# Optimization experiments

Hardware: AMD Instinct MI355X
Metric: run time of the kernel (lower is better)

## Reference

```python
import jax, jax.numpy as jnp
from jax import lax
import numpy as np

NUM_NODES = 32
C = 64
EPS = 1e-5

# Static random DAG: edge i->j (i<j) with prob 0.25; node index == topological order.
_rng = np.random.default_rng(0)
_adj = _rng.random((NUM_NODES, NUM_NODES)) < 0.25
PRED = [tuple(i for i in range(j) if _adj[i, j]) for j in range(NUM_NODES)]
SUCC = [tuple(j for j in range(i + 1, NUM_NODES) if _adj[i, j]) for i in range(NUM_NODES)]
ISPAN = [max(s) if s else NUM_NODES for s in SUCC]
# Nodes whose outputs survive the torch live/delete bookkeeping at the final stack:
# sinks (ispan == NUM_NODES) plus predecessors of the last topological node.
FINAL = [i for i in range(NUM_NODES) if ISPAN[i] >= NUM_NODES - 1]


def _sep_conv(y, dw, pw, stride):
    # depthwise 3x3 (torch padding=1) then pointwise 1x1
    y = lax.conv_general_dilated(y, dw, (stride, stride), ((1, 1), (1, 1)),
                                 feature_group_count=C,
                                 dimension_numbers=('NCHW', 'OIHW', 'NCHW'))
    return jnp.einsum('oc,nchw->nohw', pw, y)


def _bn(y, g, b, m, v):
    inv = (g / jnp.sqrt(v + EPS))[None, :, None, None]
    return (y - m[None, :, None, None]) * inv + b[None, :, None, None]


def _forward(x, dw, pw, gamma, beta, mean, var, agg_w):
    outs = [None] * NUM_NODES
    for i in range(NUM_NODES):  # static structural loop over the fixed DAG
        preds = PRED[i]
        if len(preds) == 0:          # input node: consumes x, downsample stride 2
            y, stride = x, 2
        elif len(preds) == 1:        # single predecessor: plain pass-through (squeeze)
            y, stride = outs[preds[0]], 1
        else:                         # sigmoid-weighted sum of predecessor outputs
            w = jax.nn.sigmoid(agg_w[i, :len(preds)])
            y = jnp.einsum('pnchw,p->nchw', jnp.stack([outs[p] for p in preds]), w)
            stride = 1
        h = _sep_conv(jax.nn.relu(y), dw[i], pw[i], stride)
        outs[i] = _bn(h, gamma[i], beta[i], mean[i], var[i])
    return jnp.mean(jnp.stack([outs[i] for i in FINAL]), axis=0)


def setup_inputs():
    key = jax.random.key(0)
    ks = jax.random.split(key, 8)
    B, H, W = 8, 112, 112
    x = jax.random.normal(ks[0], (B, C, H, W), jnp.float32)
    # fan-in scaling keeps activations bounded across the up-to-32-deep DAG
    dw = jax.random.normal(ks[1], (NUM_NODES, C, 1, 3, 3), jnp.float32) / 3.0
    pw = jax.random.normal(ks[2], (NUM_NODES, C, C), jnp.float32) / 8.0
    gamma = jax.random.uniform(ks[3], (NUM_NODES, C), jnp.float32, 0.5, 1.5)
    beta = jax.random.normal(ks[4], (NUM_NODES, C), jnp.float32) * 0.1
    mean = jax.random.normal(ks[5], (NUM_NODES, C), jnp.float32) * 0.1
    var = jax.random.uniform(ks[6], (NUM_NODES, C), jnp.float32, 0.5, 1.5)
    agg_w = jax.random.normal(ks[7], (NUM_NODES, NUM_NODES), jnp.float32)
    return {"x": x, "dw": dw, "pw": pw, "gamma": gamma, "beta": beta,
            "mean": mean, "var": var, "agg_w": agg_w}


def reference(x, dw, pw, gamma, beta, mean, var, agg_w):
    return _forward(x, dw, pw, gamma, beta, mean, var, agg_w)
```

## Files before the change

### kernel.cpp

```cpp
#include <hip/hip_runtime.h>
#include <cstdint>
#include <cstddef>

#define NN 32
#define NODE_ELEMS 1605632

typedef unsigned __int128 u128;
typedef __attribute__((ext_vector_type(8))) short bf16x8;
typedef __attribute__((ext_vector_type(4))) float f32x4;

static void compute_adj(bool adj[NN][NN]) {
  uint32_t pool[4];
  uint32_t hc = 0x43b0d7e5u;
  auto hashmix = [&hc](uint32_t v) -> uint32_t {
    v ^= hc; hc *= 0x931e8875u; v *= hc; v ^= v >> 16; return v;
  };
  auto mix = [](uint32_t x, uint32_t y) -> uint32_t {
    uint32_t r = x * 0xca01f9ddu - y * 0x4973f715u; r ^= r >> 16; return r;
  };
  for (int i = 0; i < 4; i++) pool[i] = hashmix(0u);
  for (int s = 0; s < 4; s++)
    for (int d = 0; d < 4; d++)
      if (s != d) pool[d] = mix(pool[d], hashmix(pool[s]));
  uint32_t hb = 0x8b51f9ddu;
  uint32_t w[8];
  for (int k = 0; k < 8; k++) {
    uint32_t v = pool[k & 3];
    v ^= hb; hb *= 0x58f38dedu; v *= hb; v ^= v >> 16;
    w[k] = v;
  }
  uint64_t s64[4];
  for (int j = 0; j < 4; j++) s64[j] = (uint64_t)w[2 * j] | ((uint64_t)w[2 * j + 1] << 32);
  u128 initstate = ((u128)s64[0] << 64) | s64[1];
  u128 initseq   = ((u128)s64[2] << 64) | s64[3];
  const u128 MULT = ((u128)0x2360ED051FC65DA4ULL << 64) | 0x4385DF649FCCF645ULL;
  u128 state = 0;
  u128 inc = (initseq << 1) | 1;
  state = state * MULT + inc;
  state += initstate;
  state = state * MULT + inc;
  for (int i = 0; i < NN; i++)
    for (int j = 0; j < NN; j++) {
      state = state * MULT + inc;
      uint64_t hi = (uint64_t)(state >> 64), lo = (uint64_t)state;
      unsigned rot = (unsigned)(hi >> 58);
      uint64_t xr = hi ^ lo;
      uint64_t out = (xr >> rot) | (xr << ((64u - rot) & 63u));
      double dv = (double)(out >> 11) * (1.0 / 9007199254740992.0);
      adj[i][j] = (dv < 0.25);
    }
}

struct NodeDesc {
  uint8_t node, npred, slot, flags;
  uint8_t pred_slot[31];
  uint8_t pad;
};
struct GroupArg { int n; NodeDesc d[32]; };
struct FinalArg { int nf; uint8_t slot[32]; };

__device__ __forceinline__ float bf2f_lo(unsigned int w) {
  union { unsigned int u; float f; } c; c.u = w << 16; return c.f;
}
__device__ __forceinline__ float bf2f_hi(unsigned int w) {
  union { unsigned int u; float f; } c; c.u = w & 0xFFFF0000u; return c.f;
}
__device__ __forceinline__ float bf2f(unsigned short h) {
  union { unsigned int u; float f; } c; c.u = ((unsigned int)h) << 16; return c.f;
}
__device__ __forceinline__ unsigned short f2bf(float f) {
  union { float f; unsigned int u; } c; c.f = f;
  unsigned int u = c.u + 0x7FFFu + ((c.u >> 16) & 1u);
  return (unsigned short)(u >> 16);
}

__global__ void prep_kernel(const float* __restrict__ pwall,
                            const float* __restrict__ aggw,
                            unsigned short* __restrict__ pwswz,
                            float* __restrict__ wsig) {
  int i = blockIdx.x * 256 + threadIdx.x;
  if (i < NN * 4096) {
    int cc = i & 63, o = (i >> 6) & 63;
    int base = i & ~4095;
    pwswz[base + o * 64 + ((((cc >> 3) ^ (o & 7)) << 3) | (cc & 7))] = f2bf(pwall[i]);
  } else {
    int j = i - NN * 4096;
    if (j < NN * NN) wsig[j] = 1.f / (1.f + expf(-aggw[j]));
  }
}

__global__ __launch_bounds__(256) void input_kernel(
    GroupArg g,
    const float* __restrict__ x,
    const float* __restrict__ dwall,
    const unsigned short* __restrict__ pwswz,
    const float* __restrict__ gmall,
    const float* __restrict__ btall,
    const float* __restrict__ mnall,
    const float* __restrict__ vrall,
    unsigned short* __restrict__ wsb)
{
  __shared__ float xtile[5 * 17 * 64];
  __shared__ __align__(16) unsigned short tbuf[1024];

  const int b = blockIdx.x & 7;
  const int m = blockIdx.x >> 3;
  const int t = threadIdx.x;
  const int ty = (m / 7) * 2;
  const int tx = (m % 7) * 8;

  const int dwc = t & 63;
  const int pbase = (t >> 6) * 4;

  {
    const int r0 = t >> 6;
    const float* xb = x + (size_t)(b * 64 + dwc) * 12544;
    const int iy0 = ty * 2 - 1;
    const int xbase = tx * 2 - 4;
    for (int iyL = r0; iyL < 5; iyL += 4) {
      int gy = iy0 + iyL;
      bool rowok = ((unsigned)gy < 112u);
      const float* row = xb + gy * 112 + xbase;
      float4 z = make_float4(0.f, 0.f, 0.f, 0.f);
      float4 v0 = z, v1 = z, v2 = z, v3 = z, v4 = z;
      if (rowok) {
        if (xbase >= 0) v0 = *(const float4*)(row);
        v1 = *(const float4*)(row + 4);
        v2 = *(const float4*)(row + 8);
        v3 = *(const float4*)(row + 12);
        v4 = *(const float4*)(row + 16);
      }
      float* dst = xtile + (iyL * 17) * 64 + dwc;
      dst[0 * 64]  = fmaxf(v0.w, 0.f);
      dst[1 * 64]  = fmaxf(v1.x, 0.f);
      dst[2 * 64]  = fmaxf(v1.y, 0.f);
      dst[3 * 64]  = fmaxf(v1.z, 0.f);
      dst[4 * 64]  = fmaxf(v1.w, 0.f);
      dst[5 * 64]  = fmaxf(v2.x, 0.f);
      dst[6 * 64]  = fmaxf(v2.y, 0.f);
      dst[7 * 64]  = fmaxf(v2.z, 0.f);
      dst[8 * 64]  = fmaxf(v2.w, 0.f);
      dst[9 * 64]  = fmaxf(v3.x, 0.f);
      dst[10 * 64] = fmaxf(v3.y, 0.f);
      dst[11 * 64] = fmaxf(v3.z, 0.f);
      dst[12 * 64] = fmaxf(v3.w, 0.f);
      dst[13 * 64] = fmaxf(v4.x, 0.f);
      dst[14 * 64] = fmaxf(v4.y, 0.f);
      dst[15 * 64] = fmaxf(v4.z, 0.f);
      dst[16 * 64] = fmaxf(v4.w, 0.f);
    }
  }

  const int lane = t & 63;
  const int wave = t >> 6;
  const int lm = lane & 15;
  const int quad = lane >> 4;
  const int oc = wave * 16 + lm;

  float kk9[9];
  {
    const float* k9 = dwall + (g.d[0].node * 64 + dwc) * 9;
    #pragma unroll
    for (int q = 0; q < 9; q++) kk9[q] = k9[q];
  }

  for (int kk = 0; kk < g.n; kk++) {
    const NodeDesc nd = g.d[kk];
    const int node = nd.node;

    __syncthreads();

    const unsigned short* pwn = pwswz + node * 4096;
    bf16x8 bfrag[2];
    #pragma unroll
    for (int ks = 0; ks < 2; ks++) {
      int gg = ks * 4 + quad;
      bfrag[ks] = *(const bf16x8*)&pwn[oc * 64 + ((gg ^ (oc & 7)) << 3)];
    }

    float tv[4];
    #pragma unroll
    for (int jj = 0; jj < 4; jj++) {
      int p = pbase + jj;
      int py = p >> 3, px = p & 7;
      const float* r0 = xtile + ((py * 2) * 17 + px * 2) * 64 + dwc;
      tv[jj] = r0[0]    * kk9[0] + r0[64]   * kk9[1] + r0[128]  * kk9[2]
             + r0[1088] * kk9[3] + r0[1152] * kk9[4] + r0[1216] * kk9[5]
             + r0[2176] * kk9[6] + r0[2240] * kk9[7] + r0[2304] * kk9[8];
    }

    #pragma unroll
    for (int jj = 0; jj < 4; jj++) {
      int p = pbase + jj;
      tbuf[p * 64 + ((((dwc >> 3) ^ (p & 7)) << 3) | (dwc & 7))] = f2bf(tv[jj]);
    }

    float nk9[9];
    if (kk + 1 < g.n) {
      const float* k9 = dwall + (g.d[kk + 1].node * 64 + dwc) * 9;
      #pragma unroll
      for (int q = 0; q < 9; q++) nk9[q] = k9[q];
    }

    __syncthreads();

    bf16x8 afrag[2];
    #pragma unroll
    for (int ks = 0; ks < 2; ks++) {
      int pos = lm;
      int gg = ks * 4 + quad;
      afrag[ks] = *(const bf16x8*)&tbuf[pos * 64 + ((gg ^ (pos & 7)) << 3)];
    }
    f32x4 acc = (f32x4){0.f, 0.f, 0.f, 0.f};
    #pragma unroll
    for (int ks = 0; ks < 2; ks++)
      acc = __builtin_amdgcn_mfma_f32_16x16x32_bf16(afrag[ks], bfrag[ks], acc, 0, 0, 0);

    unsigned short* slotp = wsb + (size_t)nd.slot * NODE_ELEMS;
    {
      int gi = node * 64 + oc;
      float inv = gmall[gi] / sqrtf(vrall[gi] + 1e-5f);
      float mn = mnall[gi], btv = btall[gi];
      #pragma unroll
      for (int rr = 0; rr < 4; rr++) {
        int pos = quad * 4 + rr;
        int gy = ty + (pos >> 3), gx = tx + (pos & 7);
        size_t base = (((size_t)(b * 56 + gy)) * 56 + gx) * 64 + oc;
        slotp[base] = f2bf((acc[rr] - mn) * inv + btv);
      }
    }

    if (kk + 1 < g.n) {
      #pragma unroll
      for (int q = 0; q < 9; q++) kk9[q] = nk9[q];
    }
  }
}

__global__ __launch_bounds__(256) void level_kernel(
    GroupArg g,
    const float* __restrict__ dwall,
    const unsigned short* __restrict__ pwswz,
    const float* __restrict__ gmall,
    const float* __restrict__ btall,
    const float* __restrict__ mnall,
    const float* __restrict__ vrall,
    const float* __restrict__ wsig,
    unsigned short* __restrict__ wsb)
{
  __shared__ float smem[3840];
  __shared__ __align__(16) unsigned short tbuf[2048];

  const int bid = blockIdx.x;
  const int nid = bid / 784;
  const int r   = bid - nid * 784;
  const int b = r & 7;
  const int m = r >> 3;
  const int t = threadIdx.x;
  const int ty = (m / 7) * 4;
  const int tx = (m % 7) * 8;

  const NodeDesc nd = g.d[nid];
  const int node = nd.node;

  const int dwc = t & 63;
  const int pbase = (t >> 6) * 8;

  const int lane = t & 63;
  const int wave = t >> 6;
  const int mtile = wave & 1;
  const int npair = wave >> 1;
  const int lm = lane & 15;
  const int quad = lane >> 4;
  const unsigned short* pwn = pwswz + node * 4096;
  bf16x8 bfrag[2][2];
  #pragma unroll
  for (int nt = 0; nt < 2; nt++) {
    int oc = (npair * 2 + nt) * 16 + lm;
    #pragma unroll
    for (int ks = 0; ks < 2; ks++) {
      int gg = ks * 4 + quad;
      bfrag[nt][ks] = *(const bf16x8*)&pwn[oc * 64 + ((gg ^ (oc & 7)) << 3)];
    }
  }

  const float* k9 = dwall + (node * 64 + dwc) * 9;
  float kk9[9];
  #pragma unroll
  for (int q = 0; q < 9; q++) kk9[q] = k9[q];

  const int np = nd.npred;
  float sa[2][8];
  int off[2];
  bool inb[2];
  #pragma unroll
  for (int u = 0; u < 2; u++) {
    int idx = t + u * 256;
    bool valid = (u == 0) || (t < 224);
    int pos = idx >> 3, q8 = idx & 7;
    int hy = pos / 10, hx = pos - hy * 10;
    int gy = ty + hy - 1, gx = tx + hx - 1;
    inb[u] = valid && ((unsigned)gy < 56u) && ((unsigned)gx < 56u);
    off[u] = ((b * 56 + gy) * 56 + gx) * 64 + q8 * 8;
    #pragma unroll
    for (int q = 0; q < 8; q++) sa[u][q] = 0.f;
  }
  for (int p0 = 0; p0 < np; p0 += 4) {
    uint4 v[4][2];
    #pragma unroll
    for (int pp = 0; pp < 4; pp++) {
      if (p0 + pp < np) {
        const unsigned short* pb = wsb + (size_t)nd.pred_slot[p0 + pp] * NODE_ELEMS;
        #pragma unroll
        for (int u = 0; u < 2; u++)
          if (inb[u]) v[pp][u] = *(const uint4*)(pb + off[u]);
      }
    }
    float wv4[4];
    #pragma unroll
    for (int pp = 0; pp < 4; pp++)
      if (p0 + pp < np)
        wv4[pp] = (np == 1) ? 1.0f : wsig[node * 32 + p0 + pp];
    #pragma unroll
    for (int pp = 0; pp < 4; pp++) {
      if (p0 + pp < np) {
        float wv = wv4[pp];
        #pragma unroll
        for (int u = 0; u < 2; u++) {
          if (inb[u]) {
            sa[u][0] = fmaf(wv, bf2f_lo(v[pp][u].x), sa[u][0]);
            sa[u][1] = fmaf(wv, bf2f_hi(v[pp][u].x), sa[u][1]);
            sa[u][2] = fmaf(wv, bf2f_lo(v[pp][u].y), sa[u][2]);
            sa[u][3] = fmaf(wv, bf2f_hi(v[pp][u].y), sa[u][3]);
            sa[u][4] = fmaf(wv, bf2f_lo(v[pp][u].z), sa[u][4]);
            sa[u][5] = fmaf(wv, bf2f_hi(v[pp][u].z), sa[u][5]);
            sa[u][6] = fmaf(wv, bf2f_lo(v[pp][u].w), sa[u][6]);
            sa[u][7] = fmaf(wv, bf2f_hi(v[pp][u].w), sa[u][7]);
          }
        }
      }
    }
  }
  #pragma unroll
  for (int u = 0; u < 2; u++) {
    int idx = t + u * 256;
    if ((u == 0) || (t < 224)) {
      float4 s0 = make_float4(fmaxf(sa[u][0], 0.f), fmaxf(sa[u][1], 0.f),
                              fmaxf(sa[u][2], 0.f), fmaxf(sa[u][3], 0.f));
      float4 s1 = make_float4(fmaxf(sa[u][4], 0.f), fmaxf(sa[u][5], 0.f),
                              fmaxf(sa[u][6], 0.f), fmaxf(sa[u][7], 0.f));
      *(float4*)&smem[idx * 8] = s0;
      *(float4*)&smem[idx * 8 + 4] = s1;
    }
  }
  __syncthreads();
  float tv[8];
  #pragma unroll
  for (int jj = 0; jj < 8; jj++) {
    int p = pbase + jj;
    int py = p >> 3, px = p & 7;
    const float* r0 = smem + (py * 10 + px) * 64 + dwc;
    tv[jj] = r0[0]    * kk9[0] + r0[64]   * kk9[1] + r0[128]  * kk9[2]
           + r0[640]  * kk9[3] + r0[704]  * kk9[4] + r0[768]  * kk9[5]
           + r0[1280] * kk9[6] + r0[1344] * kk9[7] + r0[1408] * kk9[8];
  }

  #pragma unroll
  for (int jj = 0; jj < 8; jj++) {
    int p = pbase + jj;
    tbuf[p * 64 + ((((dwc >> 3) ^ (p & 7)) << 3) | (dwc & 7))] = f2bf(tv[jj]);
  }
  __syncthreads();

  bf16x8 afrag[2];
  #pragma unroll
  for (int ks = 0; ks < 2; ks++) {
    int pos = mtile * 16 + lm;
    int gg = ks * 4 + quad;
    afrag[ks] = *(const bf16x8*)&tbuf[pos * 64 + ((gg ^ (pos & 7)) << 3)];
  }
  f32x4 acc[2];
  #pragma unroll
  for (int nt = 0; nt < 2; nt++) {
    acc[nt] = (f32x4){0.f, 0.f, 0.f, 0.f};
    #pragma unroll
    for (int ks = 0; ks < 2; ks++)
      acc[nt] = __builtin_amdgcn_mfma_f32_16x16x32_bf16(afrag[ks], bfrag[nt][ks], acc[nt], 0, 0, 0);
  }

  unsigned short* slotp = wsb + (size_t)nd.slot * NODE_ELEMS;
  #pragma unroll
  for (int nt = 0; nt < 2; nt++) {
    int oc = (npair * 2 + nt) * 16 + lm;
    int gi = node * 64 + oc;
    float inv = gmall[gi] / sqrtf(vrall[gi] + 1e-5f);
    float mn = mnall[gi], btv = btall[gi];
    #pragma unroll
    for (int rr = 0; rr < 4; rr++) {
      int pos = mtile * 16 + quad * 4 + rr;
      int gy = ty + (pos >> 3), gx = tx + (pos & 7);
      size_t base = (((size_t)(b * 56 + gy)) * 56 + gx) * 64 + oc;
      slotp[base] = f2bf((acc[nt][rr] - mn) * inv + btv);
    }
  }
}

__global__ __launch_bounds__(256) void chain_kernel(
    GroupArg g,
    const float* __restrict__ dwall,
    const unsigned short* __restrict__ pwswz,
    const float* __restrict__ gmall,
    const float* __restrict__ btall,
    const float* __restrict__ mnall,
    const float* __restrict__ vrall,
    const float* __restrict__ wsig,
    unsigned short* __restrict__ wsb)
{
  __shared__ float smem[2560];
  __shared__ __align__(16) unsigned short tbuf[1024];

  const int bid = blockIdx.x;
  const int b = bid & 7;
  const int m = bid >> 3;
  const int t = threadIdx.x;
  const int ty = (m / 7) * 2;
  const int tx = (m % 7) * 8;

  const NodeDesc nd = g.d[0];
  const int node = nd.node;

  const int dwc = t & 63;
  const int pbase = (t >> 6) * 4;

  const int lane = t & 63;
  const int wave = t >> 6;
  const int lm = lane & 15;
  const int quad = lane >> 4;
  const int oc = wave * 16 + lm;
  const unsigned short* pwn = pwswz + node * 4096;
  bf16x8 bfrag[2];
  #pragma unroll
  for (int ks = 0; ks < 2; ks++) {
    int gg = ks * 4 + quad;
    bfrag[ks] = *(const bf16x8*)&pwn[oc * 64 + ((gg ^ (oc & 7)) << 3)];
  }

  const float* k9 = dwall + (node * 64 + dwc) * 9;
  float kk9[9];
  #pragma unroll
  for (int q = 0; q < 9; q++) kk9[q] = k9[q];

  const int np = nd.npred;
  float sa[2][8];
  int off[2];
  bool inb[2];
  #pragma unroll
  for (int u = 0; u < 2; u++) {
    int idx = t + u * 256;
    bool valid = (u == 0) || (t < 64);
    int pos = idx >> 3, q8 = idx & 7;
    int hy = pos / 10, hx = pos - hy * 10;
    int gy = ty + hy - 1, gx = tx + hx - 1;
    inb[u] = valid && ((unsigned)gy < 56u) && ((unsigned)gx < 56u);
    off[u] = ((b * 56 + gy) * 56 + gx) * 64 + q8 * 8;
    #pragma unroll
    for (int q = 0; q < 8; q++) sa[u][q] = 0.f;
  }
  for (int p0 = 0; p0 < np; p0 += 4) {
    uint4 v[4][2];
    #pragma unroll
    for (int pp = 0; pp < 4; pp++) {
      if (p0 + pp < np) {
        const unsigned short* pb = wsb + (size_t)nd.pred_slot[p0 + pp] * NODE_ELEMS;
        #pragma unroll
        for (int u = 0; u < 2; u++)
          if (inb[u]) v[pp][u] = *(const uint4*)(pb + off[u]);
      }
    }
    float wv4[4];
    #pragma unroll
    for (int pp = 0; pp < 4; pp++)
      if (p0 + pp < np)
        wv4[pp] = (np == 1) ? 1.0f : wsig[node * 32 + p0 + pp];
    #pragma unroll
    for (int pp = 0; pp < 4; pp++) {
      if (p0 + pp < np) {
        float wv = wv4[pp];
        #pragma unroll
        for (int u = 0; u < 2; u++) {
          if (inb[u]) {
            sa[u][0] = fmaf(wv, bf2f_lo(v[pp][u].x), sa[u][0]);
            sa[u][1] = fmaf(wv, bf2f_hi(v[pp][u].x), sa[u][1]);
            sa[u][2] = fmaf(wv, bf2f_lo(v[pp][u].y), sa[u][2]);
            sa[u][3] = fmaf(wv, bf2f_hi(v[pp][u].y), sa[u][3]);
            sa[u][4] = fmaf(wv, bf2f_lo(v[pp][u].z), sa[u][4]);
            sa[u][5] = fmaf(wv, bf2f_hi(v[pp][u].z), sa[u][5]);
            sa[u][6] = fmaf(wv, bf2f_lo(v[pp][u].w), sa[u][6]);
            sa[u][7] = fmaf(wv, bf2f_hi(v[pp][u].w), sa[u][7]);
          }
        }
      }
    }
  }
  #pragma unroll
  for (int u = 0; u < 2; u++) {
    int idx = t + u * 256;
    if ((u == 0) || (t < 64)) {
      float4 s0 = make_float4(fmaxf(sa[u][0], 0.f), fmaxf(sa[u][1], 0.f),
                              fmaxf(sa[u][2], 0.f), fmaxf(sa[u][3], 0.f));
      float4 s1 = make_float4(fmaxf(sa[u][4], 0.f), fmaxf(sa[u][5], 0.f),
                              fmaxf(sa[u][6], 0.f), fmaxf(sa[u][7], 0.f));
      *(float4*)&smem[idx * 8] = s0;
      *(float4*)&smem[idx * 8 + 4] = s1;
    }
  }
  __syncthreads();
  float tv[4];
  #pragma unroll
  for (int jj = 0; jj < 4; jj++) {
    int p = pbase + jj;
    int py = p >> 3, px = p & 7;
    const float* r0 = smem + (py * 10 + px) * 64 + dwc;
    tv[jj] = r0[0]    * kk9[0] + r0[64]   * kk9[1] + r0[128]  * kk9[2]
           + r0[640]  * kk9[3] + r0[704]  * kk9[4] + r0[768]  * kk9[5]
           + r0[1280] * kk9[6] + r0[1344] * kk9[7] + r0[1408] * kk9[8];
  }

  #pragma unroll
  for (int jj = 0; jj < 4; jj++) {
    int p = pbase + jj;
    tbuf[p * 64 + ((((dwc >> 3) ^ (p & 7)) << 3) | (dwc & 7))] = f2bf(tv[jj]);
  }
  __syncthreads();

  bf16x8 afrag[2];
  #pragma unroll
  for (int ks = 0; ks < 2; ks++) {
    int pos = lm;
    int gg = ks * 4 + quad;
    afrag[ks] = *(const bf16x8*)&tbuf[pos * 64 + ((gg ^ (pos & 7)) << 3)];
  }
  f32x4 acc = (f32x4){0.f, 0.f, 0.f, 0.f};
  #pragma unroll
  for (int ks = 0; ks < 2; ks++)
    acc = __builtin_amdgcn_mfma_f32_16x16x32_bf16(afrag[ks], bfrag[ks], acc, 0, 0, 0);

  unsigned short* slotp = wsb + (size_t)nd.slot * NODE_ELEMS;
  {
    int gi = node * 64 + oc;
    float inv = gmall[gi] / sqrtf(vrall[gi] + 1e-5f);
    float mn = mnall[gi], btv = btall[gi];
    #pragma unroll
    for (int rr = 0; rr < 4; rr++) {
      int pos = quad * 4 + rr;
      int gy = ty + (pos >> 3), gx = tx + (pos & 7);
      size_t base = (((size_t)(b * 56 + gy)) * 56 + gx) * 64 + oc;
      slotp[base] = f2bf((acc[rr] - mn) * inv + btv);
    }
  }
}

__global__ __launch_bounds__(256) void finalize_kernel(
    FinalArg fa, const unsigned short* __restrict__ wsb,
    float* __restrict__ out, float inv_nf)
{
  __shared__ float lds[64 * 29];
  const int bid = blockIdx.x;
  const int half = bid & 1;
  const int by = bid >> 1;
  const int b = by / 56, y = by - b * 56;
  const int x0 = half * 28;
  const size_t rbase = ((((size_t)b * 56 + y) * 56) + x0) * 64;
  const int t = threadIdx.x;
  const int nf = fa.nf;

  if (t < 224) {
    const int xx = t >> 3, q8 = t & 7;
    const unsigned short* p0 = wsb + rbase + xx * 64 + q8 * 8;
    float s0 = 0.f, s1 = 0.f, s2 = 0.f, s3 = 0.f,
          s4 = 0.f, s5 = 0.f, s6 = 0.f, s7 = 0.f;
    for (int f0 = 0; f0 < nf; f0 += 4) {
      uint4 va, vb, vc, vd;
      if (f0 + 0 < nf) va = *(const uint4*)(p0 + (size_t)fa.slot[f0 + 0] * NODE_ELEMS);
      if (f0 + 1 < nf) vb = *(const uint4*)(p0 + (size_t)fa.slot[f0 + 1] * NODE_ELEMS);
      if (f0 + 2 < nf) vc = *(const uint4*)(p0 + (size_t)fa.slot[f0 + 2] * NODE_ELEMS);
      if (f0 + 3 < nf) vd = *(const uint4*)(p0 + (size_t)fa.slot[f0 + 3] * NODE_ELEMS);
      if (f0 + 0 < nf) {
        s0 += bf2f_lo(va.x); s1 += bf2f_hi(va.x); s2 += bf2f_lo(va.y); s3 += bf2f_hi(va.y);
        s4 += bf2f_lo(va.z); s5 += bf2f_hi(va.z); s6 += bf2f_lo(va.w); s7 += bf2f_hi(va.w);
      }
      if (f0 + 1 < nf) {
        s0 += bf2f_lo(vb.x); s1 += bf2f_hi(vb.x); s2 += bf2f_lo(vb.y); s3 += bf2f_hi(vb.y);
        s4 += bf2f_lo(vb.z); s5 += bf2f_hi(vb.z); s6 += bf2f_lo(vb.w); s7 += bf2f_hi(vb.w);
      }
      if (f0 + 2 < nf) {
        s0 += bf2f_lo(vc.x); s1 += bf2f_hi(vc.x); s2 += bf2f_lo(vc.y); s3 += bf2f_hi(vc.y);
        s4 += bf2f_lo(vc.z); s5 += bf2f_hi(vc.z); s6 += bf2f_lo(vc.w); s7 += bf2f_hi(vc.w);
      }
      if (f0 + 3 < nf) {
        s0 += bf2f_lo(vd.x); s1 += bf2f_hi(vd.x); s2 += bf2f_lo(vd.y); s3 += bf2f_hi(vd.y);
        s4 += bf2f_lo(vd.z); s5 += bf2f_hi(vd.z); s6 += bf2f_lo(vd.w); s7 += bf2f_hi(vd.w);
      }
    }
    float* dl = lds + (q8 * 8) * 29 + xx;
    dl[0 * 29] = s0 * inv_nf; dl[1 * 29] = s1 * inv_nf;
    dl[2 * 29] = s2 * inv_nf; dl[3 * 29] = s3 * inv_nf;
    dl[4 * 29] = s4 * inv_nf; dl[5 * 29] = s5 * inv_nf;
    dl[6 * 29] = s6 * inv_nf; dl[7 * 29] = s7 * inv_nf;
  }
  __syncthreads();
  float* dst = out + (size_t)b * 64 * 3136 + (size_t)y * 56 + x0;
  for (int j = t; j < 1792; j += 256) {
    int c = j / 28, xx = j - c * 28;
    dst[(size_t)c * 3136 + xx] = lds[c * 29 + xx];
  }
}

extern "C" void kernel_launch(void* const* d_in, const int* in_sizes, int n_in,
                              void* d_out, int out_size, void* d_ws, size_t ws_size,
                              hipStream_t stream) {
  (void)in_sizes; (void)n_in; (void)ws_size; (void)out_size;
  const float* x     = (const float*)d_in[0];
  const float* dw    = (const float*)d_in[1];
  const float* pw    = (const float*)d_in[2];
  const float* gamma = (const float*)d_in[3];
  const float* beta  = (const float*)d_in[4];
  const float* mean  = (const float*)d_in[5];
  const float* var   = (const float*)d_in[6];
  const float* aggw  = (const float*)d_in[7];
  unsigned short* wsb = (unsigned short*)d_ws;
  float* out = (float*)d_out;

  bool adj[NN][NN];
  compute_adj(adj);

  int npred[NN], preds[NN][NN], nsucc[NN], ispan[NN], level[NN];
  for (int j = 0; j < NN; j++) {
    npred[j] = 0;
    for (int i = 0; i < j; i++) if (adj[i][j]) preds[j][npred[j]++] = i;
  }
  for (int i = 0; i < NN; i++) {
    nsucc[i] = 0; ispan[i] = NN;
    int mx = -1;
    for (int j = i + 1; j < NN; j++) if (adj[i][j]) { nsucc[i]++; mx = j; }
    if (nsucc[i] > 0) ispan[i] = mx;
  }
  int maxlev = 0;
  for (int j = 0; j < NN; j++) {
    int lv = 0;
    for (int p = 0; p < npred[j]; p++) {
      int cand = level[preds[j][p]] + 1;
      if (cand > lv) lv = cand;
    }
    level[j] = lv;
    if (lv > maxlev) maxlev = lv;
  }
  bool isfinal[NN]; int nf = 0;
  for (int i = 0; i < NN; i++) { isfinal[i] = (ispan[i] >= NN - 1); if (isfinal[i]) nf++; }
  int lastlvl[NN];
  for (int i = 0; i < NN; i++) {
    lastlvl[i] = -1;
    for (int j = i + 1; j < NN; j++) if (adj[i][j] && level[j] > lastlvl[i]) lastlvl[i] = level[j];
  }
  int slot[NN]; bool used[NN];
  for (int s = 0; s < NN; s++) used[s] = false;
  for (int L = 0; L <= maxlev; L++) {
    for (int i = 0; i < NN; i++) {
      if (level[i] != L) continue;
      int s = 0; while (used[s]) s++;
      used[s] = true; slot[i] = s;
    }
    for (int i = 0; i < NN; i++)
      if (level[i] <= L && !isfinal[i] && lastlvl[i] == L)
        used[slot[i]] = false;
  }
  int maxs = 0;
  for (int i = 0; i < NN; i++) if (slot[i] > maxs) maxs = slot[i];

  unsigned short* pwswz = wsb + (size_t)(maxs + 1) * NODE_ELEMS;
  float* wsig = (float*)(pwswz + NN * 4096);

  float inv_nf = 1.0f / (float)nf;

  prep_kernel<<<516, 256, 0, stream>>>(pw, aggw, pwswz, wsig);

  for (int L = 0; L <= maxlev; L++) {
    GroupArg g; g.n = 0;
    for (int i = 0; i < NN; i++) {
      if (level[i] != L) continue;
      NodeDesc& nd = g.d[g.n++];
      nd.node = (uint8_t)i;
      nd.npred = (uint8_t)npred[i];
      nd.slot = (uint8_t)slot[i];
      nd.flags = 0;
      for (int p = 0; p < npred[i]; p++) nd.pred_slot[p] = (uint8_t)slot[preds[i][p]];
    }
    if (g.n > 0) {
      if (L == 0) {
        input_kernel<<<1568, 256, 0, stream>>>(g, x, dw, pwswz, gamma, beta,
                                               mean, var, wsb);
      } else if (g.n == 1) {
        chain_kernel<<<1568, 256, 0, stream>>>(g, dw, pwswz, gamma, beta,
                                               mean, var, wsig, wsb);
      } else {
        level_kernel<<<784 * g.n, 256, 0, stream>>>(g, dw, pwswz, gamma, beta,
                                                    mean, var, wsig, wsb);
      }
    }
  }

  FinalArg fa; fa.nf = 0;
  for (int i = 0; i < NN; i++) if (isfinal[i]) fa.slot[fa.nf++] = (uint8_t)slot[i];
  finalize_kernel<<<896, 256, 0, stream>>>(fa, wsb, out, inv_nf);
}
```

Before: 222.9 us.

## Fuse last DAG node computation with final mean-stack into one kernel

When the deepest level has a single node and that node is a final output, the new kernel computes that node and immediately averages it with the other final node outputs, writing NCHW fp32 output directly. This removes one kernel launch, plus the write and re-read of the last node's activation through global memory. In exchange the fused kernel's output writes are scattered 8-wide tile rows instead of 28-wide rows. The finalize loop is also simplified from 4-way unrolled loads to a plain loop.

```diff
diff --git a/kernel.cpp b/kernel.cpp
--- a/kernel.cpp
+++ b/kernel.cpp
@@ -560,6 +560,196 @@
   }
 }
 
+__global__ __launch_bounds__(256) void chain_final_kernel(
+    GroupArg g, FinalArg fa, int fself,
+    const float* __restrict__ dwall,
+    const unsigned short* __restrict__ pwswz,
+    const float* __restrict__ gmall,
+    const float* __restrict__ btall,
+    const float* __restrict__ mnall,
+    const float* __restrict__ vrall,
+    const float* __restrict__ wsig,
+    const unsigned short* __restrict__ wsb,
+    float* __restrict__ out, float inv_nf)
+{
+  __shared__ float smem[2560];
+  __shared__ __align__(16) unsigned short tbuf[1024];
+
+  const int bid = blockIdx.x;
+  const int b = bid & 7;
+  const int m = bid >> 3;
+  const int t = threadIdx.x;
+  const int ty = (m / 7) * 2;
+  const int tx = (m % 7) * 8;
+
+  const NodeDesc nd = g.d[0];
+  const int node = nd.node;
+
+  const int dwc = t & 63;
+  const int pbase = (t >> 6) * 4;
+
+  const int lane = t & 63;
+  const int wave = t >> 6;
+  const int lm = lane & 15;
+  const int quad = lane >> 4;
+  const int oc = wave * 16 + lm;
+  const unsigned short* pwn = pwswz + node * 4096;
+  bf16x8 bfrag[2];
+  #pragma unroll
+  for (int ks = 0; ks < 2; ks++) {
+    int gg = ks * 4 + quad;
+    bfrag[ks] = *(const bf16x8*)&pwn[oc * 64 + ((gg ^ (oc & 7)) << 3)];
+  }
+
+  const float* k9 = dwall + (node * 64 + dwc) * 9;
+  float kk9[9];
+  #pragma unroll
+  for (int q = 0; q < 9; q++) kk9[q] = k9[q];
+
+  const int np = nd.npred;
+  float sa[2][8];
+  int off[2];
+  bool inb[2];
+  #pragma unroll
+  for (int u = 0; u < 2; u++) {
+    int idx = t + u * 256;
+    bool valid = (u == 0) || (t < 64);
+    int pos = idx >> 3, q8 = idx & 7;
+    int hy = pos / 10, hx = pos - hy * 10;
+    int gy = ty + hy - 1, gx = tx + hx - 1;
+    inb[u] = valid && ((unsigned)gy < 56u) && ((unsigned)gx < 56u);
+    off[u] = ((b * 56 + gy) * 56 + gx) * 64 + q8 * 8;
+    #pragma unroll
+    for (int q = 0; q < 8; q++) sa[u][q] = 0.f;
+  }
+  for (int p0 = 0; p0 < np; p0 += 4) {
+    uint4 v[4][2];
+    #pragma unroll
+    for (int pp = 0; pp < 4; pp++) {
+      if (p0 + pp < np) {
+        const unsigned short* pb = wsb + (size_t)nd.pred_slot[p0 + pp] * NODE_ELEMS;
+        #pragma unroll
+        for (int u = 0; u < 2; u++)
+          if (inb[u]) v[pp][u] = *(const uint4*)(pb + off[u]);
+      }
+    }
+    float wv4[4];
+    #pragma unroll
+    for (int pp = 0; pp < 4; pp++)
+      if (p0 + pp < np)
+        wv4[pp] = (np == 1) ? 1.0f : wsig[node * 32 + p0 + pp];
+    #pragma unroll
+    for (int pp = 0; pp < 4; pp++) {
+      if (p0 + pp < np) {
+        float wv = wv4[pp];
+        #pragma unroll
+        for (int u = 0; u < 2; u++) {
+          if (inb[u]) {
+            sa[u][0] = fmaf(wv, bf2f_lo(v[pp][u].x), sa[u][0]);
+            sa[u][1] = fmaf(wv, bf2f_hi(v[pp][u].x), sa[u][1]);
+            sa[u][2] = fmaf(wv, bf2f_lo(v[pp][u].y), sa[u][2]);
+            sa[u][3] = fmaf(wv, bf2f_hi(v[pp][u].y), sa[u][3]);
+            sa[u][4] = fmaf(wv, bf2f_lo(v[pp][u].z), sa[u][4]);
+            sa[u][5] = fmaf(wv, bf2f_hi(v[pp][u].z), sa[u][5]);
+            sa[u][6] = fmaf(wv, bf2f_lo(v[pp][u].w), sa[u][6]);
+            sa[u][7] = fmaf(wv, bf2f_hi(v[pp][u].w), sa[u][7]);
+          }
+        }
+      }
+    }
+  }
+  #pragma unroll
+  for (int u = 0; u < 2; u++) {
+    int idx = t + u * 256;
+    if ((u == 0) || (t < 64)) {
+      float4 s0 = make_float4(fmaxf(sa[u][0], 0.f), fmaxf(sa[u][1], 0.f),
+                              fmaxf(sa[u][2], 0.f), fmaxf(sa[u][3], 0.f));
+      float4 s1 = make_float4(fmaxf(sa[u][4], 0.f), fmaxf(sa[u][5], 0.f),
+                              fmaxf(sa[u][6], 0.f), fmaxf(sa[u][7], 0.f));
+      *(float4*)&smem[idx * 8] = s0;
+      *(float4*)&smem[idx * 8 + 4] = s1;
+    }
+  }
+  __syncthreads();
+  float tv[4];
+  #pragma unroll
+  for (int jj = 0; jj < 4; jj++) {
+    int p = pbase + jj;
+    int py = p >> 3, px = p & 7;
+    const float* r0 = smem + (py * 10 + px) * 64 + dwc;
+    tv[jj] = r0[0]    * kk9[0] + r0[64]   * kk9[1] + r0[128]  * kk9[2]
+           + r0[640]  * kk9[3] + r0[704]  * kk9[4] + r0[768]  * kk9[5]
+           + r0[1280] * kk9[6] + r0[1344] * kk9[7] + r0[1408] * kk9[8];
+  }
+
+  #pragma unroll
+  for (int jj = 0; jj < 4; jj++) {
+    int p = pbase + jj;
+    tbuf[p * 64 + ((((dwc >> 3) ^ (p & 7)) << 3) | (dwc & 7))] = f2bf(tv[jj]);
+  }
+  __syncthreads();
+
+  bf16x8 afrag[2];
+  #pragma unroll
+  for (int ks = 0; ks < 2; ks++) {
+    int pos = lm;
+    int gg = ks * 4 + quad;
+    afrag[ks] = *(const bf16x8*)&tbuf[pos * 64 + ((gg ^ (pos & 7)) << 3)];
+  }
+  f32x4 acc = (f32x4){0.f, 0.f, 0.f, 0.f};
+  #pragma unroll
+  for (int ks = 0; ks < 2; ks++)
+    acc = __builtin_amdgcn_mfma_f32_16x16x32_bf16(afrag[ks], bfrag[ks], acc, 0, 0, 0);
+
+  unsigned short own[4];
+  {
+    int gi = node * 64 + oc;
+    float inv = gmall[gi] / sqrtf(vrall[gi] + 1e-5f);
+    float mn = mnall[gi], btv = btall[gi];
+    #pragma unroll
+    for (int rr = 0; rr < 4; rr++)
+      own[rr] = f2bf((acc[rr] - mn) * inv + btv);
+  }
+  __syncthreads();
+  #pragma unroll
+  for (int rr = 0; rr < 4; rr++)
+    tbuf[(quad * 4 + rr) * 64 + oc] = own[rr];
+  __syncthreads();
+
+  if (t < 128) {
+    int pos = t >> 3, q8 = t & 7;
+    int gy = ty + (pos >> 3), gx = tx + (pos & 7);
+    size_t base = (((size_t)(b * 56 + gy)) * 56 + gx) * 64 + q8 * 8;
+    float s0 = 0.f, s1 = 0.f, s2 = 0.f, s3 = 0.f,
+          s4 = 0.f, s5 = 0.f, s6 = 0.f, s7 = 0.f;
+    for (int f = 0; f < fa.nf; f++) {
+      if (f == fself) {
+        const unsigned short* op = &tbuf[pos * 64 + q8 * 8];
+        s0 += bf2f(op[0]); s1 += bf2f(op[1]); s2 += bf2f(op[2]); s3 += bf2f(op[3]);
+        s4 += bf2f(op[4]); s5 += bf2f(op[5]); s6 += bf2f(op[6]); s7 += bf2f(op[7]);
+      } else {
+        uint4 v = *(const uint4*)(wsb + (size_t)fa.slot[f] * NODE_ELEMS + base);
+        s0 += bf2f_lo(v.x); s1 += bf2f_hi(v.x); s2 += bf2f_lo(v.y); s3 += bf2f_hi(v.y);
+        s4 += bf2f_lo(v.z); s5 += bf2f_hi(v.z); s6 += bf2f_lo(v.w); s7 += bf2f_hi(v.w);
+      }
+    }
+    float* fb = smem + (q8 * 8) * 17 + pos;
+    fb[0 * 17] = s0 * inv_nf; fb[1 * 17] = s1 * inv_nf;
+    fb[2 * 17] = s2 * inv_nf; fb[3 * 17] = s3 * inv_nf;
+    fb[4 * 17] = s4 * inv_nf; fb[5 * 17] = s5 * inv_nf;
+    fb[6 * 17] = s6 * inv_nf; fb[7 * 17] = s7 * inv_nf;
+  }
+  __syncthreads();
+  {
+    float* dst = out + (size_t)b * 64 * 3136;
+    for (int j = t; j < 1024; j += 256) {
+      int c = j >> 4, pos = j & 15;
+      int gy = ty + (pos >> 3), gx = tx + (pos & 7);
+      dst[(size_t)c * 3136 + gy * 56 + gx] = smem[c * 17 + pos];
+    }
+  }
+}
+
 __global__ __launch_bounds__(256) void finalize_kernel(
     FinalArg fa, const unsigned short* __restrict__ wsb,
     float* __restrict__ out, float inv_nf)
@@ -579,28 +769,10 @@
     const unsigned short* p0 = wsb + rbase + xx * 64 + q8 * 8;
     float s0 = 0.f, s1 = 0.f, s2 = 0.f, s3 = 0.f,
           s4 = 0.f, s5 = 0.f, s6 = 0.f, s7 = 0.f;
-    for (int f0 = 0; f0 < nf; f0 += 4) {
-      uint4 va, vb, vc, vd;
-      if (f0 + 0 < nf) va = *(const uint4*)(p0 + (size_t)fa.slot[f0 + 0] * NODE_ELEMS);
-      if (f0 + 1 < nf) vb = *(const uint4*)(p0 + (size_t)fa.slot[f0 + 1] * NODE_ELEMS);
-      if (f0 + 2 < nf) vc = *(const uint4*)(p0 + (size_t)fa.slot[f0 + 2] * NODE_ELEMS);
-      if (f0 + 3 < nf) vd = *(const uint4*)(p0 + (size_t)fa.slot[f0 + 3] * NODE_ELEMS);
-      if (f0 + 0 < nf) {
-        s0 += bf2f_lo(va.x); s1 += bf2f_hi(va.x); s2 += bf2f_lo(va.y); s3 += bf2f_hi(va.y);
-        s4 += bf2f_lo(va.z); s5 += bf2f_hi(va.z); s6 += bf2f_lo(va.w); s7 += bf2f_hi(va.w);
-      }
-      if (f0 + 1 < nf) {
-        s0 += bf2f_lo(vb.x); s1 += bf2f_hi(vb.x); s2 += bf2f_lo(vb.y); s3 += bf2f_hi(vb.y);
-        s4 += bf2f_lo(vb.z); s5 += bf2f_hi(vb.z); s6 += bf2f_lo(vb.w); s7 += bf2f_hi(vb.w);
-      }
-      if (f0 + 2 < nf) {
-        s0 += bf2f_lo(vc.x); s1 += bf2f_hi(vc.x); s2 += bf2f_lo(vc.y); s3 += bf2f_hi(vc.y);
-        s4 += bf2f_lo(vc.z); s5 += bf2f_hi(vc.z); s6 += bf2f_lo(vc.w); s7 += bf2f_hi(vc.w);
-      }
-      if (f0 + 3 < nf) {
-        s0 += bf2f_lo(vd.x); s1 += bf2f_hi(vd.x); s2 += bf2f_lo(vd.y); s3 += bf2f_hi(vd.y);
-        s4 += bf2f_lo(vd.z); s5 += bf2f_hi(vd.z); s6 += bf2f_lo(vd.w); s7 += bf2f_hi(vd.w);
-      }
+    for (int f = 0; f < nf; f++) {
+      uint4 v = *(const uint4*)(p0 + (size_t)fa.slot[f] * NODE_ELEMS);
+      s0 += bf2f_lo(v.x); s1 += bf2f_hi(v.x); s2 += bf2f_lo(v.y); s3 += bf2f_hi(v.y);
+      s4 += bf2f_lo(v.z); s5 += bf2f_hi(v.z); s6 += bf2f_lo(v.w); s7 += bf2f_hi(v.w);
     }
     float* dl = lds + (q8 * 8) * 29 + xx;
     dl[0 * 29] = s0 * inv_nf; dl[1 * 29] = s1 * inv_nf;
@@ -682,6 +854,16 @@
 
   float inv_nf = 1.0f / (float)nf;
 
+  int lastN = -1, lastCount = 0;
+  for (int i = 0; i < NN; i++) if (level[i] == maxlev) { lastN = i; lastCount++; }
+  bool fuse = (maxlev >= 1) && (lastCount == 1) && isfinal[lastN];
+  FinalArg fa; fa.nf = 0; int fself = -1;
+  for (int i = 0; i < NN; i++) if (isfinal[i]) {
+    if (i == lastN) fself = fa.nf;
+    fa.slot[fa.nf++] = (uint8_t)slot[i];
+  }
+  if (fself < 0) fuse = false;
+
   prep_kernel<<<516, 256, 0, stream>>>(pw, aggw, pwswz, wsig);
 
   for (int L = 0; L <= maxlev; L++) {
@@ -699,6 +881,10 @@
       if (L == 0) {
         input_kernel<<<1568, 256, 0, stream>>>(g, x, dw, pwswz, gamma, beta,
                                                mean, var, wsb);
+      } else if (L == maxlev && fuse) {
+        chain_final_kernel<<<1568, 256, 0, stream>>>(g, fa, fself, dw, pwswz,
+                                                     gamma, beta, mean, var,
+                                                     wsig, wsb, out, inv_nf);
       } else if (g.n == 1) {
         chain_kernel<<<1568, 256, 0, stream>>>(g, dw, pwswz, gamma, beta,
                                                mean, var, wsig, wsb);
@@ -709,7 +895,7 @@
     }
   }
 
-  FinalArg fa; fa.nf = 0;
-  for (int i = 0; i < NN; i++) if (isfinal[i]) fa.slot[fa.nf++] = (uint8_t)slot[i];
-  finalize_kernel<<<896, 256, 0, stream>>>(fa, wsb, out, inv_nf);
-}
+  if (!fuse) {
+    finalize_kernel<<<896, 256, 0, stream>>>(fa, wsb, out, inv_nf);
+  }
+}
```

After: 223.6 us. Within noise of the previous version (+0.3%).
